# Kernel tuning notes

Measured on AMD Instinct MI355X. Metric: run time of the kernel, lower is better.

## Reference

```python
import jax, jax.numpy as jnp
import numpy as np

NUM_HEADS = 8
KEY_DIM = 16
D = 32          # attn_ratio * key_dim
DH = D * NUM_HEADS  # 256
NH_KD = KEY_DIM * NUM_HEADS  # 128
DIM = 256


def _conv1x1_bn(x, W, s, b):
    # 1x1 conv (no bias) followed by eval-mode BatchNorm folded to affine.
    # x: [B, Cin, H, W], W: [Cout, Cin], s/b: [Cout]
    y = jnp.einsum('oc,bchw->bohw', W, x)
    return y * s[None, :, None, None] + b[None, :, None, None]


def setup_inputs() -> dict:
    key = jax.random.key(0)
    ks = jax.random.split(key, 16)
    B, C, H, Wd = 2, DIM, 64, 64
    rgb = jax.random.normal(ks[0], (B, C, H, Wd), dtype=jnp.float32)
    edge = jax.random.normal(ks[1], (B, C, H, Wd), dtype=jnp.float32)

    def conv_w(k, o, i):
        return jax.random.normal(k, (o, i), dtype=jnp.float32) * (1.0 / np.sqrt(i))

    def bn(k, c):
        k1, k2 = jax.random.split(k)
        s = jax.random.uniform(k1, (c,), dtype=jnp.float32, minval=0.5, maxval=1.5)
        b = jax.random.normal(k2, (c,), dtype=jnp.float32) * 0.1
        return s, b

    Wq = conv_w(ks[2], NH_KD, C); sq, bq = bn(ks[3], NH_KD)
    Wk = conv_w(ks[4], NH_KD, C); sk, bk = bn(ks[5], NH_KD)
    Wv = conv_w(ks[6], DH, C);   sv, bv = bn(ks[7], DH)
    Wp = conv_w(ks[8], C, DH);   sp, bp = bn(ks[9], C)
    return dict(rgb=rgb, edge=edge, Wq=Wq, sq=sq, bq=bq, Wk=Wk, sk=sk, bk=bk,
                Wv=Wv, sv=sv, bv=bv, Wp=Wp, sp=sp, bp=bp)


def reference(rgb, edge, Wq, sq, bq, Wk, sk, bk, Wv, sv, bv, Wp, sp, bp):
    B, C, H, Wd = rgb.shape
    N = H * Wd
    # Q from rgb, K/V from edge (all 1x1 conv + BN)
    qq = _conv1x1_bn(rgb, Wq, sq, bq).reshape(B, NUM_HEADS, KEY_DIM, N)
    qq = jnp.transpose(qq, (0, 1, 3, 2))                       # [B,h,N,kd]
    kk = _conv1x1_bn(edge, Wk, sk, bk).reshape(B, NUM_HEADS, KEY_DIM, N)  # [B,h,kd,N]
    vv = _conv1x1_bn(edge, Wv, sv, bv).reshape(B, NUM_HEADS, D, N)
    vv = jnp.transpose(vv, (0, 1, 3, 2))                       # [B,h,N,d]
    # NOTE: original forward does NOT apply self.scale -- faithful omission.
    attn = jnp.einsum('bhnk,bhkm->bhnm', qq, kk)               # [B,h,N,N]
    attn = jax.nn.softmax(attn, axis=-1)
    xx = jnp.einsum('bhnm,bhmd->bhnd', attn, vv)               # [B,h,N,d]
    xx = jnp.transpose(xx, (0, 1, 3, 2)).reshape(B, DH, H, Wd)
    xx = jax.nn.relu(xx)                                       # activation before proj conv
    xx = _conv1x1_bn(xx, Wp, sp, bp)                           # [B,C,H,W]
    return xx
```

## Files before the change

kernel.cpp:

```cpp
#include <hip/hip_runtime.h>
#include <hip/hip_bf16.h>

#define NB 2
#define CIN 256
#define NPIX 4096
#define NHEADS 8
#define KD 16
#define DV 32
#define DH 256
#define NHKD 128

typedef short bf16x8 __attribute__((ext_vector_type(8)));
typedef short s16x4 __attribute__((ext_vector_type(4)));
typedef float f32x2 __attribute__((ext_vector_type(2)));
typedef float f32x4 __attribute__((ext_vector_type(4)));
typedef float f32x16 __attribute__((ext_vector_type(16)));
typedef unsigned int u32x2 __attribute__((ext_vector_type(2)));
typedef unsigned int u32x4 __attribute__((ext_vector_type(4)));

#define LOG2E 1.4426950408889634f

static __device__ __forceinline__ unsigned short f2bf(float f) {
    __hip_bfloat16 h = __float2bfloat16(f);
    return __builtin_bit_cast(unsigned short, h);
}

__global__ __launch_bounds__(256) void k_prep(
    const float* __restrict__ Wq, const float* __restrict__ Wk,
    const float* __restrict__ Wv, const float* __restrict__ Wp,
    unsigned short* __restrict__ wq, unsigned short* __restrict__ wk,
    unsigned short* __restrict__ wv, unsigned short* __restrict__ wp)
{
    int i = blockIdx.x * 256 + threadIdx.x;
    if (i < NHKD * CIN) { wq[i] = f2bf(Wq[i]); wk[i] = f2bf(Wk[i]); }
    if (i < DH * CIN)   { wv[i] = f2bf(Wv[i]); wp[i] = f2bf(Wp[i]); }
}

__global__ __launch_bounds__(256) void k_qkv(
    const float* __restrict__ rgb, const float* __restrict__ edge,
    const unsigned short* __restrict__ wq, const unsigned short* __restrict__ wk,
    const unsigned short* __restrict__ wv,
    const float* __restrict__ sq, const float* __restrict__ bq,
    const float* __restrict__ sk, const float* __restrict__ bk,
    const float* __restrict__ sv, const float* __restrict__ bv,
    unsigned short* __restrict__ Qw, unsigned short* __restrict__ Kw,
    unsigned short* __restrict__ Vw)
{
    const int nb = blockIdx.x;
    const int ob = blockIdx.y;
    const int b  = blockIdx.z;
    const int tid = threadIdx.x;
    const int wave = tid >> 6, lane = tid & 63;
    const int cl = lane & 15, g = lane >> 4;

    const float* X; const unsigned short* W; const float* sc; const float* bi;
    int obase, job;
    if (ob < 2)      { X = rgb  + (size_t)b*CIN*NPIX; W = wq; sc = sq; bi = bq; obase = ob*64;     job = 0; }
    else if (ob < 4) { X = edge + (size_t)b*CIN*NPIX; W = wk; sc = sk; bi = bk; obase = (ob-2)*64; job = 1; }
    else             { X = edge + (size_t)b*CIN*NPIX; W = wv; sc = sv; bi = bv; obase = (ob-4)*64; job = 2; }

    __shared__ float xt[32 * 65];

    f32x4 acc[4];
    #pragma unroll
    for (int i = 0; i < 4; i++) acc[i] = (f32x4)0.f;

    const int n0 = nb * 64;
    const int ow = obase + wave * 16 + cl;
    const unsigned short* Wrow = W + (size_t)ow * CIN;

    for (int kt = 0; kt < 8; kt++) {
        __syncthreads();
        {
            int tr = tid >> 6;
            int tc = tid & 63;
            #pragma unroll
            for (int r = 0; r < 8; r++) {
                int c_local = r * 4 + tr;
                xt[c_local * 65 + tc] = X[(size_t)(kt * 32 + c_local) * NPIX + n0 + tc];
            }
        }
        __syncthreads();
        #pragma unroll
        for (int ns = 0; ns < 4; ns++) {
            bf16x8 a;
            #pragma unroll
            for (int j = 0; j < 8; j++)
                a[j] = (short)f2bf(xt[(8 * g + j) * 65 + ns * 16 + cl]);
            bf16x8 wfrag = *reinterpret_cast<const bf16x8*>(Wrow + kt * 32 + 8 * g);
            acc[ns] = __builtin_amdgcn_mfma_f32_16x16x32_bf16(a, wfrag, acc[ns], 0, 0, 0);
        }
    }

    const float sco = sc[ow], bio = bi[ow];
    if (job == 2) {
        int h = ow >> 5, d = ow & 31;
        unsigned short* dst = Vw + ((size_t)((b * 8 + h) * 32 + d)) * NPIX;
        #pragma unroll
        for (int ns = 0; ns < 4; ns++) {
            int nr = n0 + ns * 16 + 4 * g;
            s16x4 pk;
            #pragma unroll
            for (int r = 0; r < 4; r++) pk[r] = (short)f2bf(acc[ns][r] * sco + bio);
            *reinterpret_cast<s16x4*>(dst + nr) = pk;
        }
    } else {
        float scq = sco, biq = bio;
        if (job == 0) { scq *= LOG2E; biq *= LOG2E; }
        unsigned short* base = (job == 0) ? Qw : Kw;
        int h = ow >> 4, kd = ow & 15;
        unsigned short* dst = base + ((size_t)(b * 8 + h) * NPIX) * KD + kd;
        #pragma unroll
        for (int ns = 0; ns < 4; ns++)
            #pragma unroll
            for (int r = 0; r < 4; r++) {
                int nr = n0 + ns * 16 + 4 * g + r;
                dst[(size_t)nr * KD] = f2bf(acc[ns][r] * scq + biq);
            }
    }
}

typedef const unsigned int __attribute__((address_space(1)))* gp_t;
typedef unsigned int __attribute__((address_space(3)))* lp_t;

__global__ __launch_bounds__(256) void k_attn(
    const unsigned short* __restrict__ Qw, const unsigned short* __restrict__ Kw,
    const unsigned short* __restrict__ Vw, unsigned short* __restrict__ Ow)
{
    const int qg = blockIdx.x;
    const int bh = blockIdx.y;
    const int tid = threadIdx.x;
    const int wave = tid >> 6, lane = tid & 63;
    const int l31 = lane & 31, hi = lane >> 5;

    __shared__ union {
        unsigned short v[4][2][2048];
        struct { float o[4][32][32]; float l[4][32]; } c;
    } sh;

    const unsigned short* Kbase = Kw + (size_t)bh * NPIX * KD;
    const unsigned short* Vbase = Vw + (size_t)bh * DV * NPIX;

    const int q0 = qg * 32;
    const bf16x8 qf = *(const bf16x8*)(Qw + ((size_t)bh * NPIX + q0 + l31) * KD + 8 * hi);

    const unsigned short* Kln = Kbase + (size_t)l31 * KD + 8 * hi;
#define KF0(T) (*(const bf16x8*)(Kln + ((T) * 64 + 0) * KD))
#define KF1(T) (*(const bf16x8*)(Kln + ((T) * 64 + 32) * KD))

    const int scb = ((lane & 7) * 16) ^ ((lane >> 3) << 4);
    const unsigned short* Vln = Vbase + (size_t)(lane >> 3) * NPIX + (scb >> 1);
#define STAGE(T, BUF) do { _Pragma("unroll") for (int j = 0; j < 4; ++j) \
    __builtin_amdgcn_global_load_lds( \
        (gp_t)(const void*)(Vln + (size_t)j * 8 * NPIX + (size_t)(T) * 64), \
        (lp_t)(void*)(&sh.v[wave][BUF][j * 512]), 16, 0, 0); } while (0)

    const int vsw = (l31 & 7) << 4;

    f32x16 o = (f32x16)0.f;
    float l_run = 0.f;
    const f32x16 z16 = (f32x16)0.f;

    const int T0 = wave * 16;
    bf16x8 ka0 = KF0(T0), ka1 = KF1(T0);
    bf16x8 kb0, kb1;
    STAGE(T0, 0);

    #pragma unroll
    for (int t = 0; t < 16; ++t) {
        const int T = T0 + t;
        const int cur = t & 1;
        if (t < 15) {
            kb0 = KF0(T + 1);
            kb1 = KF1(T + 1);
            STAGE(T + 1, cur ^ 1);
        }

        f32x16 s0 = __builtin_amdgcn_mfma_f32_32x32x16_bf16(ka0, qf, z16, 0, 0, 0);
        f32x16 s1 = __builtin_amdgcn_mfma_f32_32x32x16_bf16(ka1, qf, z16, 0, 0, 0);
        #pragma unroll
        for (int i = 0; i < 16; ++i) s0[i] = __builtin_amdgcn_exp2f(s0[i]);
        #pragma unroll
        for (int i = 0; i < 16; ++i) s1[i] = __builtin_amdgcn_exp2f(s1[i]);

        f32x2 r[8];
        #pragma unroll
        for (int i = 0; i < 8; ++i) {
            f32x2 a = {s0[2*i], s0[2*i+1]};
            f32x2 b = {s1[2*i], s1[2*i+1]};
            r[i] = a + b;
        }
        r[0] += r[4]; r[1] += r[5]; r[2] += r[6]; r[3] += r[7];
        r[0] += r[2]; r[1] += r[3];
        r[0] += r[1];
        l_run += r[0].x + r[0].y;

        unsigned up[16];
        #pragma unroll
        for (int ss = 0; ss < 8; ++ss) {
            up[ss]     = (unsigned)f2bf(s0[2*ss]) | ((unsigned)f2bf(s0[2*ss+1]) << 16);
            up[8 + ss] = (unsigned)f2bf(s1[2*ss]) | ((unsigned)f2bf(s1[2*ss+1]) << 16);
        }
        #pragma unroll
        for (int gg = 0; gg < 4; ++gg) {
            u32x2 r0 = __builtin_amdgcn_permlane32_swap(up[4*gg+0], up[4*gg+2], false, false);
            up[4*gg+0] = r0.x; up[4*gg+2] = r0.y;
            u32x2 r1 = __builtin_amdgcn_permlane32_swap(up[4*gg+1], up[4*gg+3], false, false);
            up[4*gg+1] = r1.x; up[4*gg+3] = r1.y;
        }

        asm volatile("s_waitcnt vmcnt(0)" ::: "memory");

        #pragma unroll
        for (int c = 0; c < 4; ++c) {
            u32x4 av;
            av.x = up[4*c + 0];
            av.y = up[4*c + 1];
            av.z = up[4*c + 2];
            av.w = up[4*c + 3];
            const int vidx = (l31 * 128 + ((32 * c + 16 * hi) ^ vsw)) >> 1;
            bf16x8 vb = *(const bf16x8*)(&sh.v[wave][cur][vidx]);
            o = __builtin_amdgcn_mfma_f32_32x32x16_bf16(
                    __builtin_bit_cast(bf16x8, av), vb, o, 0, 0, 0);
        }
        ka0 = kb0; ka1 = kb1;
    }
#undef KF0
#undef KF1
#undef STAGE

    l_run += __shfl_xor(l_run, 32, 64);

    __syncthreads();
    #pragma unroll
    for (int r = 0; r < 16; ++r) {
        const int qr = (r & 3) + 8 * (r >> 2) + 4 * hi;
        sh.c.o[wave][qr][l31] = o[r];
    }
    if (hi == 0) sh.c.l[wave][l31] = l_run;
    __syncthreads();

    const int q = tid >> 3;
    const int d0 = (tid & 7) * 4;
    const float lsum = sh.c.l[0][q] + sh.c.l[1][q] + sh.c.l[2][q] + sh.c.l[3][q];
    const float linv = __builtin_amdgcn_rcpf(lsum);
    float v[4];
    #pragma unroll
    for (int i = 0; i < 4; ++i) {
        float s = sh.c.o[0][q][d0+i] + sh.c.o[1][q][d0+i] + sh.c.o[2][q][d0+i] + sh.c.o[3][q][d0+i];
        v[i] = fmaxf(s * linv, 0.f);
    }
    const int b = bh >> 3, h = bh & 7;
    u32x2 pk;
    pk.x = (unsigned)f2bf(v[0]) | ((unsigned)f2bf(v[1]) << 16);
    pk.y = (unsigned)f2bf(v[2]) | ((unsigned)f2bf(v[3]) << 16);
    *reinterpret_cast<u32x2*>(Ow + ((size_t)b * NPIX + q0 + q) * DH + h * DV + d0) = pk;
}

__global__ __launch_bounds__(256) void k_proj(
    const unsigned short* __restrict__ Xo, const unsigned short* __restrict__ wp,
    const float* __restrict__ sp, const float* __restrict__ bp,
    float* __restrict__ out)
{
    const int nb = blockIdx.x;
    const int b  = blockIdx.y;
    const int tid = threadIdx.x;
    const int wave = tid >> 6, lane = tid & 63;
    const int cl = lane & 15, g = lane >> 4;

    const int cbase = wave * 64;
    f32x4 acc[4][4];
    #pragma unroll
    for (int i = 0; i < 4; i++)
        #pragma unroll
        for (int j = 0; j < 4; j++) acc[i][j] = (f32x4)0.f;

    const unsigned short* Xb = Xo + ((size_t)b * NPIX + nb * 64) * DH;

    #pragma unroll
    for (int kt = 0; kt < 8; kt++) {
        bf16x8 afr[4];
        #pragma unroll
        for (int cs = 0; cs < 4; cs++)
            afr[cs] = *reinterpret_cast<const bf16x8*>(wp + (size_t)(cbase + cs * 16 + cl) * DH + kt * 32 + 8 * g);
        #pragma unroll
        for (int ns = 0; ns < 4; ns++) {
            bf16x8 bfr = *reinterpret_cast<const bf16x8*>(Xb + (size_t)(ns * 16 + cl) * DH + kt * 32 + 8 * g);
            #pragma unroll
            for (int cs = 0; cs < 4; cs++)
                acc[cs][ns] = __builtin_amdgcn_mfma_f32_16x16x32_bf16(afr[cs], bfr, acc[cs][ns], 0, 0, 0);
        }
    }

    #pragma unroll
    for (int cs = 0; cs < 4; cs++)
        #pragma unroll
        for (int r = 0; r < 4; r++) {
            int c = cbase + cs * 16 + 4 * g + r;
            float scv = sp[c], biv = bp[c];
            float* dst = out + ((size_t)b * DH + c) * NPIX + nb * 64;
            #pragma unroll
            for (int ns = 0; ns < 4; ns++)
                dst[ns * 16 + cl] = acc[cs][ns][r] * scv + biv;
        }
}

extern "C" void kernel_launch(void* const* d_in, const int* in_sizes, int n_in,
                              void* d_out, int out_size, void* d_ws, size_t ws_size,
                              hipStream_t stream) {
    const float* rgb  = (const float*)d_in[0];
    const float* edge = (const float*)d_in[1];
    const float* Wq = (const float*)d_in[2];
    const float* sq = (const float*)d_in[3];
    const float* bq = (const float*)d_in[4];
    const float* Wk = (const float*)d_in[5];
    const float* sk = (const float*)d_in[6];
    const float* bk = (const float*)d_in[7];
    const float* Wv = (const float*)d_in[8];
    const float* sv = (const float*)d_in[9];
    const float* bv = (const float*)d_in[10];
    const float* Wp = (const float*)d_in[11];
    const float* sp = (const float*)d_in[12];
    const float* bp = (const float*)d_in[13];
    float* out = (float*)d_out;

    char* ws = (char*)d_ws;
    unsigned short* wq = (unsigned short*)(ws + 0);
    unsigned short* wk = (unsigned short*)(ws + (64 << 10));
    unsigned short* wv = (unsigned short*)(ws + (128 << 10));
    unsigned short* wp = (unsigned short*)(ws + (256 << 10));
    size_t o = 384 << 10;
    unsigned short* Qw = (unsigned short*)(ws + o); o += (size_t)16 * NPIX * KD * 2;
    unsigned short* Kw = (unsigned short*)(ws + o); o += (size_t)16 * NPIX * KD * 2;
    unsigned short* Vw = (unsigned short*)(ws + o); o += (size_t)16 * DV * NPIX * 2;
    unsigned short* Ow = (unsigned short*)(ws + o);

    k_prep<<<dim3(256), dim3(256), 0, stream>>>(Wq, Wk, Wv, Wp, wq, wk, wv, wp);
    k_qkv<<<dim3(64, 8, NB), dim3(256), 0, stream>>>(rgb, edge, wq, wk, wv,
                                                     sq, bq, sk, bk, sv, bv, Qw, Kw, Vw);
    k_attn<<<dim3(128, 16), dim3(256), 0, stream>>>(Qw, Kw, Vw, Ow);
    k_proj<<<dim3(64, NB), dim3(256), 0, stream>>>(Ow, wp, sp, bp, out);
}
```

Before: 94.99 us.

## Load V directly to registers, cheaper bf16 packing, MFMA priority, smaller proj tiles

Result: slower. 101.7 us (+7.0%).

```diff
diff --git a/kernel.cpp b/kernel.cpp
--- a/kernel.cpp
+++ b/kernel.cpp
@@ -23,6 +23,12 @@
 static __device__ __forceinline__ unsigned short f2bf(float f) {
     __hip_bfloat16 h = __float2bfloat16(f);
     return __builtin_bit_cast(unsigned short, h);
+}
+
+static __device__ __forceinline__ unsigned pack_rhu(float lo, float hi) {
+    unsigned a = __builtin_bit_cast(unsigned, lo) + 0x8000u;
+    unsigned b = __builtin_bit_cast(unsigned, hi) + 0x8000u;
+    return (a >> 16) | (b & 0xffff0000u);
 }
 
 __global__ __launch_bounds__(256) void k_prep(
@@ -83,10 +89,12 @@
         __syncthreads();
         #pragma unroll
         for (int ns = 0; ns < 4; ns++) {
-            bf16x8 a;
-            #pragma unroll
-            for (int j = 0; j < 8; j++)
-                a[j] = (short)f2bf(xt[(8 * g + j) * 65 + ns * 16 + cl]);
+            u32x4 aw;
+            #pragma unroll
+            for (int w = 0; w < 4; w++)
+                aw[w] = pack_rhu(xt[(8 * g + 2 * w) * 65 + ns * 16 + cl],
+                                 xt[(8 * g + 2 * w + 1) * 65 + ns * 16 + cl]);
+            bf16x8 a = __builtin_bit_cast(bf16x8, aw);
             bf16x8 wfrag = *reinterpret_cast<const bf16x8*>(Wrow + kt * 32 + 8 * g);
             acc[ns] = __builtin_amdgcn_mfma_f32_16x16x32_bf16(a, wfrag, acc[ns], 0, 0, 0);
         }
@@ -119,9 +127,6 @@
             }
     }
 }
-
-typedef const unsigned int __attribute__((address_space(1)))* gp_t;
-typedef unsigned int __attribute__((address_space(3)))* lp_t;
 
 __global__ __launch_bounds__(256) void k_attn(
     const unsigned short* __restrict__ Qw, const unsigned short* __restrict__ Kw,
@@ -133,10 +138,7 @@
     const int wave = tid >> 6, lane = tid & 63;
     const int l31 = lane & 31, hi = lane >> 5;
 
-    __shared__ union {
-        unsigned short v[4][2][2048];
-        struct { float o[4][32][32]; float l[4][32]; } c;
-    } sh;
+    __shared__ struct { float o[4][32][32]; float l[4][32]; } sh;
 
     const unsigned short* Kbase = Kw + (size_t)bh * NPIX * KD;
     const unsigned short* Vbase = Vw + (size_t)bh * DV * NPIX;
@@ -148,14 +150,7 @@
 #define KF0(T) (*(const bf16x8*)(Kln + ((T) * 64 + 0) * KD))
 #define KF1(T) (*(const bf16x8*)(Kln + ((T) * 64 + 32) * KD))
 
-    const int scb = ((lane & 7) * 16) ^ ((lane >> 3) << 4);
-    const unsigned short* Vln = Vbase + (size_t)(lane >> 3) * NPIX + (scb >> 1);
-#define STAGE(T, BUF) do { _Pragma("unroll") for (int j = 0; j < 4; ++j) \
-    __builtin_amdgcn_global_load_lds( \
-        (gp_t)(const void*)(Vln + (size_t)j * 8 * NPIX + (size_t)(T) * 64), \
-        (lp_t)(void*)(&sh.v[wave][BUF][j * 512]), 16, 0, 0); } while (0)
-
-    const int vsw = (l31 & 7) << 4;
+    const unsigned short* Vln = Vbase + (size_t)l31 * NPIX + 8 * hi;
 
     f32x16 o = (f32x16)0.f;
     float l_run = 0.f;
@@ -164,20 +159,24 @@
     const int T0 = wave * 16;
     bf16x8 ka0 = KF0(T0), ka1 = KF1(T0);
     bf16x8 kb0, kb1;
-    STAGE(T0, 0);
 
     #pragma unroll
     for (int t = 0; t < 16; ++t) {
         const int T = T0 + t;
-        const int cur = t & 1;
+        const unsigned short* vt = Vln + T * 64;
+        bf16x8 va0 = *(const bf16x8*)(vt + 0);
+        bf16x8 va1 = *(const bf16x8*)(vt + 16);
+        bf16x8 va2 = *(const bf16x8*)(vt + 32);
+        bf16x8 va3 = *(const bf16x8*)(vt + 48);
         if (t < 15) {
             kb0 = KF0(T + 1);
             kb1 = KF1(T + 1);
-            STAGE(T + 1, cur ^ 1);
-        }
-
+        }
+
+        __builtin_amdgcn_s_setprio(1);
         f32x16 s0 = __builtin_amdgcn_mfma_f32_32x32x16_bf16(ka0, qf, z16, 0, 0, 0);
         f32x16 s1 = __builtin_amdgcn_mfma_f32_32x32x16_bf16(ka1, qf, z16, 0, 0, 0);
+        __builtin_amdgcn_s_setprio(0);
         #pragma unroll
         for (int i = 0; i < 16; ++i) s0[i] = __builtin_amdgcn_exp2f(s0[i]);
         #pragma unroll
@@ -198,8 +197,8 @@
         unsigned up[16];
         #pragma unroll
         for (int ss = 0; ss < 8; ++ss) {
-            up[ss]     = (unsigned)f2bf(s0[2*ss]) | ((unsigned)f2bf(s0[2*ss+1]) << 16);
-            up[8 + ss] = (unsigned)f2bf(s1[2*ss]) | ((unsigned)f2bf(s1[2*ss+1]) << 16);
+            up[ss]     = pack_rhu(s0[2*ss], s0[2*ss+1]);
+            up[8 + ss] = pack_rhu(s1[2*ss], s1[2*ss+1]);
         }
         #pragma unroll
         for (int gg = 0; gg < 4; ++gg) {
@@ -209,45 +208,42 @@
             up[4*gg+1] = r1.x; up[4*gg+3] = r1.y;
         }
 
-        asm volatile("s_waitcnt vmcnt(0)" ::: "memory");
-
-        #pragma unroll
-        for (int c = 0; c < 4; ++c) {
+        __builtin_amdgcn_s_setprio(1);
+        {
             u32x4 av;
-            av.x = up[4*c + 0];
-            av.y = up[4*c + 1];
-            av.z = up[4*c + 2];
-            av.w = up[4*c + 3];
-            const int vidx = (l31 * 128 + ((32 * c + 16 * hi) ^ vsw)) >> 1;
-            bf16x8 vb = *(const bf16x8*)(&sh.v[wave][cur][vidx]);
-            o = __builtin_amdgcn_mfma_f32_32x32x16_bf16(
-                    __builtin_bit_cast(bf16x8, av), vb, o, 0, 0, 0);
-        }
+            av.x = up[0]; av.y = up[1]; av.z = up[2]; av.w = up[3];
+            o = __builtin_amdgcn_mfma_f32_32x32x16_bf16(__builtin_bit_cast(bf16x8, av), va0, o, 0, 0, 0);
+            av.x = up[4]; av.y = up[5]; av.z = up[6]; av.w = up[7];
+            o = __builtin_amdgcn_mfma_f32_32x32x16_bf16(__builtin_bit_cast(bf16x8, av), va1, o, 0, 0, 0);
+            av.x = up[8]; av.y = up[9]; av.z = up[10]; av.w = up[11];
+            o = __builtin_amdgcn_mfma_f32_32x32x16_bf16(__builtin_bit_cast(bf16x8, av), va2, o, 0, 0, 0);
+            av.x = up[12]; av.y = up[13]; av.z = up[14]; av.w = up[15];
+            o = __builtin_amdgcn_mfma_f32_32x32x16_bf16(__builtin_bit_cast(bf16x8, av), va3, o, 0, 0, 0);
+        }
+        __builtin_amdgcn_s_setprio(0);
         ka0 = kb0; ka1 = kb1;
     }
 #undef KF0
 #undef KF1
-#undef STAGE
 
     l_run += __shfl_xor(l_run, 32, 64);
 
-    __syncthreads();
     #pragma unroll
     for (int r = 0; r < 16; ++r) {
         const int qr = (r & 3) + 8 * (r >> 2) + 4 * hi;
-        sh.c.o[wave][qr][l31] = o[r];
-    }
-    if (hi == 0) sh.c.l[wave][l31] = l_run;
+        sh.o[wave][qr][l31] = o[r];
+    }
+    if (hi == 0) sh.l[wave][l31] = l_run;
     __syncthreads();
 
     const int q = tid >> 3;
     const int d0 = (tid & 7) * 4;
-    const float lsum = sh.c.l[0][q] + sh.c.l[1][q] + sh.c.l[2][q] + sh.c.l[3][q];
+    const float lsum = sh.l[0][q] + sh.l[1][q] + sh.l[2][q] + sh.l[3][q];
     const float linv = __builtin_amdgcn_rcpf(lsum);
     float v[4];
     #pragma unroll
     for (int i = 0; i < 4; ++i) {
-        float s = sh.c.o[0][q][d0+i] + sh.c.o[1][q][d0+i] + sh.c.o[2][q][d0+i] + sh.c.o[3][q][d0+i];
+        float s = sh.o[0][q][d0+i] + sh.o[1][q][d0+i] + sh.o[2][q][d0+i] + sh.o[3][q][d0+i];
         v[i] = fmaxf(s * linv, 0.f);
     }
     const int b = bh >> 3, h = bh & 7;
@@ -269,13 +265,13 @@
     const int cl = lane & 15, g = lane >> 4;
 
     const int cbase = wave * 64;
-    f32x4 acc[4][4];
+    f32x4 acc[4][2];
     #pragma unroll
     for (int i = 0; i < 4; i++)
         #pragma unroll
-        for (int j = 0; j < 4; j++) acc[i][j] = (f32x4)0.f;
-
-    const unsigned short* Xb = Xo + ((size_t)b * NPIX + nb * 64) * DH;
+        for (int j = 0; j < 2; j++) acc[i][j] = (f32x4)0.f;
+
+    const unsigned short* Xb = Xo + ((size_t)b * NPIX + nb * 32) * DH;
 
     #pragma unroll
     for (int kt = 0; kt < 8; kt++) {
@@ -284,7 +280,7 @@
         for (int cs = 0; cs < 4; cs++)
             afr[cs] = *reinterpret_cast<const bf16x8*>(wp + (size_t)(cbase + cs * 16 + cl) * DH + kt * 32 + 8 * g);
         #pragma unroll
-        for (int ns = 0; ns < 4; ns++) {
+        for (int ns = 0; ns < 2; ns++) {
             bf16x8 bfr = *reinterpret_cast<const bf16x8*>(Xb + (size_t)(ns * 16 + cl) * DH + kt * 32 + 8 * g);
             #pragma unroll
             for (int cs = 0; cs < 4; cs++)
@@ -298,9 +294,9 @@
         for (int r = 0; r < 4; r++) {
             int c = cbase + cs * 16 + 4 * g + r;
             float scv = sp[c], biv = bp[c];
-            float* dst = out + ((size_t)b * DH + c) * NPIX + nb * 64;
-            #pragma unroll
-            for (int ns = 0; ns < 4; ns++)
+            float* dst = out + ((size_t)b * DH + c) * NPIX + nb * 32;
+            #pragma unroll
+            for (int ns = 0; ns < 2; ns++)
                 dst[ns * 16 + cl] = acc[cs][ns][r] * scv + biv;
         }
 }
@@ -339,5 +335,5 @@
     k_qkv<<<dim3(64, 8, NB), dim3(256), 0, stream>>>(rgb, edge, wq, wk, wv,
                                                      sq, bq, sk, bk, sv, bv, Qw, Kw, Vw);
     k_attn<<<dim3(128, 16), dim3(256), 0, stream>>>(Qw, Kw, Vw, Ow);
-    k_proj<<<dim3(64, NB), dim3(256), 0, stream>>>(Ow, wp, sp, bp, out);
-}
+    k_proj<<<dim3(128, NB), dim3(256), 0, stream>>>(Ow, wp, sp, bp, out);
+}
```
